# Kernel tuning notes

Measured on AMD Instinct MI355X. Metric: run time of the kernel, lower is better.

## Reference

```python
import jax, jax.numpy as jnp
import numpy as np

N0, N1, N2 = 819200, 81920, 8192
E1, E2 = 819200, 81920
DIN, DH, DOUT = 128, 256, 128


def setup_inputs() -> dict:
    key = jax.random.key(0)
    ks = jax.random.split(key, 12)
    inp = {
        "x": jax.random.normal(ks[0], (N0, DIN), dtype=jnp.float32),
        "src1": jax.random.randint(ks[1], (E1,), 0, N0, dtype=jnp.int32),
        "dst1": jax.random.randint(ks[2], (E1,), 0, N1, dtype=jnp.int32),
        "src2": jax.random.randint(ks[3], (E2,), 0, N1, dtype=jnp.int32),
        "dst2": jax.random.randint(ks[4], (E2,), 0, N2, dtype=jnp.int32),
        "n1": N1,
        "n2": N2,
        # SAGEConv layer 1 params (lin_l has bias, lin_r no bias, PyG default)
        "w1l": jax.random.normal(ks[5], (DIN, DH), dtype=jnp.float32) / np.sqrt(DIN),
        "b1": jnp.zeros((DH,), dtype=jnp.float32),
        "w1r": jax.random.normal(ks[6], (DIN, DH), dtype=jnp.float32) / np.sqrt(DIN),
        # SAGEConv layer 2 params
        "w2l": jax.random.normal(ks[7], (DH, DOUT), dtype=jnp.float32) / np.sqrt(DH),
        "b2": jnp.zeros((DOUT,), dtype=jnp.float32),
        "w2r": jax.random.normal(ks[8], (DH, DOUT), dtype=jnp.float32) / np.sqrt(DH),
    }
    return inp


def _sage_conv(x_src, x_dst, src, dst, n_dst, wl, bl, wr):
    # mean aggregation of neighbor (source) features into destinations
    msg = x_src[src]                                            # [E, d]
    agg = jax.ops.segment_sum(msg, dst, num_segments=n_dst)     # [n_dst, d]
    cnt = jax.ops.segment_sum(jnp.ones((dst.shape[0],), msg.dtype), dst,
                              num_segments=n_dst)               # [n_dst]
    mean = agg / jnp.maximum(cnt, 1.0)[:, None]
    return mean @ wl + bl + x_dst @ wr


def reference(x, src1, dst1, src2, dst2, n1, n2, w1l, b1, w1r, w2l, b2, w2r):
    # layer 1 (eval mode: dropout is a no-op)
    h = _sage_conv(x, x[:n1], src1, dst1, n1, w1l, b1, w1r)     # [n1, DH]
    h = jax.nn.relu(h)
    # layer 2
    out = _sage_conv(h, h[:n2], src2, dst2, n2, w2l, b2, w2r)   # [n2, DOUT]
    return out
```

## Files before the change

kernel.cpp:

```cpp
#include <hip/hip_runtime.h>

constexpr int cN0 = 819200, cN1 = 81920, cN2 = 8192;
constexpr int cE1 = 819200, cE2 = 81920;
constexpr int cDIN = 128, cDH = 256, cDOUT = 128;

typedef __attribute__((ext_vector_type(8))) short bf16x8;
typedef __attribute__((ext_vector_type(4))) float f32x4;
typedef __attribute__((ext_vector_type(8))) unsigned short u16x8;

__device__ __forceinline__ unsigned short f2bf(float f) {
    unsigned u = __builtin_bit_cast(unsigned, f);
    u += 0x7FFF + ((u >> 16) & 1);
    return (unsigned short)(u >> 16);
}
__device__ __forceinline__ float bf2f(unsigned short s) {
    unsigned u = ((unsigned)s) << 16;
    return __builtin_bit_cast(float, u);
}

__global__ __launch_bounds__(256) void hist_k(
    const int* __restrict__ dst, int* __restrict__ hist, int nedges)
{
    int e = blockIdx.x * 256 + threadIdx.x;
    if (e < nedges) atomicAdd(&hist[dst[e]], 1);
}

__global__ __launch_bounds__(1024) void partial_k(
    const int* __restrict__ a, int* __restrict__ part)
{
    const int tid = threadIdx.x, lane = tid & 63, wid = tid >> 6;
    int v = a[blockIdx.x * 1024 + tid];
    #pragma unroll
    for (int off = 32; off; off >>= 1) v += __shfl_xor(v, off);
    __shared__ int ws[16];
    if (lane == 0) ws[wid] = v;
    __syncthreads();
    if (tid == 0) {
        int s = 0;
        #pragma unroll
        for (int i = 0; i < 16; ++i) s += ws[i];
        part[blockIdx.x] = s;
    }
}

__global__ __launch_bounds__(128) void scanp_k(int* __restrict__ part)
{
    const int tid = threadIdx.x, lane = tid & 63, wid = tid >> 6;
    int v = (tid < 80) ? part[tid] : 0;
    int incl = v;
    #pragma unroll
    for (int off = 1; off < 64; off <<= 1) {
        int t = __shfl_up(incl, off, 64);
        if (lane >= off) incl += t;
    }
    __shared__ int w0;
    if (wid == 0 && lane == 63) w0 = incl;
    __syncthreads();
    int pre = wid ? w0 : 0;
    if (tid < 80) part[tid] = pre + incl - v;
}

__global__ __launch_bounds__(1024) void final_k(
    int* __restrict__ a, const int* __restrict__ part)
{
    const int tid = threadIdx.x, lane = tid & 63, wid = tid >> 6;
    const int g = blockIdx.x * 1024 + tid;
    int v = a[g];
    int incl = v;
    #pragma unroll
    for (int off = 1; off < 64; off <<= 1) {
        int t = __shfl_up(incl, off, 64);
        if (lane >= off) incl += t;
    }
    __shared__ int ws[16];
    if (lane == 63) ws[wid] = incl;
    __syncthreads();
    int pre = 0;
    #pragma unroll
    for (int i = 0; i < 16; ++i) if (i < wid) pre += ws[i];
    a[g] = part[blockIdx.x] + pre + incl - v;
}

__global__ __launch_bounds__(1024) void scan_k(int* __restrict__ a, int n)
{
    __shared__ int wsum[16];
    __shared__ int carry_s;
    const int tid = threadIdx.x;
    const int lane = tid & 63, wid = tid >> 6;
    if (tid == 0) carry_s = 0;
    __syncthreads();
    for (int base = 0; base < n; base += 1024) {
        int v = (base + tid < n) ? a[base + tid] : 0;
        int incl = v;
        #pragma unroll
        for (int off = 1; off < 64; off <<= 1) {
            int t = __shfl_up(incl, off, 64);
            if (lane >= off) incl += t;
        }
        if (lane == 63) wsum[wid] = incl;
        __syncthreads();
        int wpre = 0;
        #pragma unroll
        for (int w = 0; w < 15; ++w) if (w < wid) wpre += wsum[w];
        int c = carry_s;
        if (base + tid < n) a[base + tid] = c + wpre + incl - v;
        __syncthreads();
        if (tid == 1023) carry_s = c + wpre + incl;
    }
}

__global__ __launch_bounds__(256) void build_k(
    const int* __restrict__ src, const int* __restrict__ dst,
    int* __restrict__ cursor, int* __restrict__ eidx, int nedges)
{
    int e = blockIdx.x * 256 + threadIdx.x;
    if (e < nedges) {
        int p = atomicAdd(&cursor[dst[e]], 1);
        eidx[p] = src[e];
    }
}

__global__ __launch_bounds__(256) void agg1_k(
    const float* __restrict__ x, const int* __restrict__ cursor,
    const int* __restrict__ eidx, unsigned short* __restrict__ A1)
{
    const int row = blockIdx.x * 4 + (threadIdx.x >> 6);
    const int lane = threadIdx.x & 63;
    const int half = lane >> 5, li = lane & 31;
    const int start = row ? cursor[row - 1] : 0;
    const int end = cursor[row];
    float ax = 0.f, ay = 0.f, az = 0.f, aw = 0.f;
    for (int e = start + half; e < end; e += 2) {
        const int s = eidx[e];
        float4 v = *reinterpret_cast<const float4*>(x + (size_t)s * cDIN + li * 4);
        ax += v.x; ay += v.y; az += v.z; aw += v.w;
    }
    ax += __shfl_xor(ax, 32);
    ay += __shfl_xor(ay, 32);
    az += __shfl_xor(az, 32);
    aw += __shfl_xor(aw, 32);
    const float inv = 1.0f / fmaxf((float)(end - start), 1.0f);
    if (half == 0) {
        ushort4 o;
        o.x = f2bf(ax * inv); o.y = f2bf(ay * inv);
        o.z = f2bf(az * inv); o.w = f2bf(aw * inv);
        *reinterpret_cast<ushort4*>(A1 + (size_t)row * 256 + li * 4) = o;
    }
    float2 xv = *reinterpret_cast<const float2*>(x + (size_t)row * cDIN + lane * 2);
    unsigned pk = (unsigned)f2bf(xv.x) | ((unsigned)f2bf(xv.y) << 16);
    *reinterpret_cast<unsigned*>(A1 + (size_t)row * 256 + 128 + lane * 2) = pk;
}

__global__ __launch_bounds__(256) void agg2_k(
    const unsigned short* __restrict__ h, const int* __restrict__ cursor,
    const int* __restrict__ eidx, unsigned short* __restrict__ A2)
{
    const int row = blockIdx.x * 4 + (threadIdx.x >> 6);
    const int lane = threadIdx.x & 63;
    const int half = lane >> 5, li = lane & 31;
    const int start = row ? cursor[row - 1] : 0;
    const int end = cursor[row];
    float acc[8] = {};
    for (int e = start + half; e < end; e += 2) {
        const int s = eidx[e];
        u16x8 v = *reinterpret_cast<const u16x8*>(h + (size_t)s * cDH + li * 8);
        #pragma unroll
        for (int i = 0; i < 8; ++i) acc[i] += bf2f(v[i]);
    }
    #pragma unroll
    for (int i = 0; i < 8; ++i) acc[i] += __shfl_xor(acc[i], 32);
    const float inv = 1.0f / fmaxf((float)(end - start), 1.0f);
    if (half == 0) {
        u16x8 o;
        #pragma unroll
        for (int i = 0; i < 8; ++i) o[i] = f2bf(acc[i] * inv);
        *reinterpret_cast<u16x8*>(A2 + (size_t)row * 512 + li * 8) = o;
    }
}

__global__ __launch_bounds__(256) void wprep_k(
    const float* __restrict__ w1l, const float* __restrict__ w1r,
    const float* __restrict__ w2l, const float* __restrict__ w2r,
    unsigned short* __restrict__ W1c, unsigned short* __restrict__ W2c)
{
    int id = blockIdx.x * 256 + threadIdx.x;
    if (id < 256 * 256) {
        int n = id >> 8, k = id & 255;
        float v = (k < 128) ? w1l[k * 256 + n] : w1r[(k - 128) * 256 + n];
        W1c[n * 256 + k] = f2bf(v);
    } else {
        int id2 = id - 256 * 256;
        int n = id2 >> 9, k = id2 & 511;
        float v = (k < 256) ? w2l[k * 128 + n] : w2r[(k - 256) * 128 + n];
        W2c[n * 512 + k] = f2bf(v);
    }
}

template<int K, int N, bool L1MODE>
__global__ __launch_bounds__(256) void mfma_gemm_k(
    const unsigned short* __restrict__ A, const unsigned short* __restrict__ Bt,
    const float* __restrict__ bias,
    unsigned short* __restrict__ hout, unsigned short* __restrict__ a2r,
    float* __restrict__ fout)
{
    constexpr int LD = 40;
    __shared__ unsigned short As[128 * LD];
    __shared__ unsigned short Bs[128 * LD];

    const int tid = threadIdx.x;
    const int l = tid & 63, w = tid >> 6;
    const int q = l >> 4, r16 = l & 15;
    const int wr0 = (w >> 1) * 64, wc0 = (w & 1) * 64;
    const int n0 = blockIdx.x * 128, row0 = blockIdx.y * 128;

    const f32x4 zero = {0.f, 0.f, 0.f, 0.f};
    f32x4 acc[4][4];
    #pragma unroll
    for (int m = 0; m < 4; ++m)
        #pragma unroll
        for (int n = 0; n < 4; ++n) acc[m][n] = zero;

    for (int k0 = 0; k0 < K; k0 += 32) {
        __syncthreads();
        #pragma unroll
        for (int c = 0; c < 2; ++c) {
            int z = tid + c * 256;
            int r = z >> 2, o16 = z & 3;
            bf16x8 av = *reinterpret_cast<const bf16x8*>(A + (size_t)(row0 + r) * K + k0 + o16 * 8);
            bf16x8 bv = *reinterpret_cast<const bf16x8*>(Bt + (size_t)(n0 + r) * K + k0 + o16 * 8);
            *reinterpret_cast<bf16x8*>(As + r * LD + o16 * 8) = av;
            *reinterpret_cast<bf16x8*>(Bs + r * LD + o16 * 8) = bv;
        }
        __syncthreads();
        bf16x8 af[4], bg[4];
        #pragma unroll
        for (int m = 0; m < 4; ++m)
            af[m] = *reinterpret_cast<const bf16x8*>(As + (wr0 + 16 * m + r16) * LD + q * 8);
        #pragma unroll
        for (int n = 0; n < 4; ++n)
            bg[n] = *reinterpret_cast<const bf16x8*>(Bs + (wc0 + 16 * n + r16) * LD + q * 8);
        #pragma unroll
        for (int m = 0; m < 4; ++m)
            #pragma unroll
            for (int n = 0; n < 4; ++n)
                acc[m][n] = __builtin_amdgcn_mfma_f32_16x16x32_bf16(af[m], bg[n], acc[m][n], 0, 0, 0);
    }

    #pragma unroll
    for (int n = 0; n < 4; ++n) {
        const int col = n0 + wc0 + 16 * n + r16;
        const float bv = bias[col];
        #pragma unroll
        for (int m = 0; m < 4; ++m) {
            #pragma unroll
            for (int j = 0; j < 4; ++j) {
                const int row = row0 + wr0 + 16 * m + 4 * q + j;
                float v = acc[m][n][j] + bv;
                if (L1MODE) {
                    v = fmaxf(v, 0.f);
                    unsigned short b = f2bf(v);
                    hout[(size_t)row * N + col] = b;
                    if (row < cN2) a2r[(size_t)row * 512 + col] = b;
                } else {
                    fout[(size_t)row * N + col] = v;
                }
            }
        }
    }
}

extern "C" void kernel_launch(void* const* d_in, const int* in_sizes, int n_in,
                              void* d_out, int out_size, void* d_ws, size_t ws_size,
                              hipStream_t stream)
{
    const float* x    = (const float*)d_in[0];
    const int*   src1 = (const int*)d_in[1];
    const int*   dst1 = (const int*)d_in[2];
    const int*   src2 = (const int*)d_in[3];
    const int*   dst2 = (const int*)d_in[4];
    const float* w1l  = (const float*)d_in[7];
    const float* b1   = (const float*)d_in[8];
    const float* w1r  = (const float*)d_in[9];
    const float* w2l  = (const float*)d_in[10];
    const float* b2   = (const float*)d_in[11];
    const float* w2r  = (const float*)d_in[12];
    float* out = (float*)d_out;

    unsigned short* A1  = (unsigned short*)d_ws;
    unsigned short* h   = A1 + (size_t)cN1 * 256;
    unsigned short* A2  = h + (size_t)cN1 * 256;
    unsigned short* W1c = A2 + (size_t)cN2 * 512;
    unsigned short* W2c = W1c + 256 * 256;
    int* offs1 = (int*)(W2c + 128 * 512);
    int* eidx1 = offs1 + cN1;
    int* offs2 = eidx1 + cE1;
    int* eidx2 = offs2 + cN2;
    int* part1 = eidx2 + cE2;

    hipMemsetAsync(offs1, 0, (size_t)cN1 * sizeof(int), stream);
    hipMemsetAsync(offs2, 0, (size_t)cN2 * sizeof(int), stream);

    wprep_k<<<(256 * 256 + 128 * 512) / 256, 256, 0, stream>>>(w1l, w1r, w2l, w2r, W1c, W2c);

    hist_k<<<cE1 / 256, 256, 0, stream>>>(dst1, offs1, cE1);
    partial_k<<<cN1 / 1024, 1024, 0, stream>>>(offs1, part1);
    scanp_k<<<1, 128, 0, stream>>>(part1);
    final_k<<<cN1 / 1024, 1024, 0, stream>>>(offs1, part1);
    build_k<<<cE1 / 256, 256, 0, stream>>>(src1, dst1, offs1, eidx1, cE1);
    agg1_k<<<cN1 / 4, 256, 0, stream>>>(x, offs1, eidx1, A1);

    mfma_gemm_k<256, 256, true><<<dim3(2, cN1 / 128), 256, 0, stream>>>(
        A1, W1c, b1, h, A2 + 256, nullptr);

    hist_k<<<cE2 / 256, 256, 0, stream>>>(dst2, offs2, cE2);
    scan_k<<<1, 1024, 0, stream>>>(offs2, cN2);
    build_k<<<cE2 / 256, 256, 0, stream>>>(src2, dst2, offs2, eidx2, cE2);
    agg2_k<<<cN2 / 4, 256, 0, stream>>>(h, offs2, eidx2, A2);

    mfma_gemm_k<512, 128, false><<<dim3(1, cN2 / 128), 256, 0, stream>>>(
        A2, W2c, b2, nullptr, nullptr, out);
}
```

Before: 280.7 us.

## Merge both graph CSR builds and feed GEMMs from split left/right sources

The CSR construction for both layers now runs in one pass. A single offsets array covers both layers, and the histogram, scan and build kernels handle both edge sets together, with the memsets folded into the weight-prep kernel. This removes the serial single-block scan and several launches. The GEMMs no longer need concatenated A buffers: the left half is read from the bf16 mean and the right half directly from x (converted from fp32 on load) or from h. Layer 2 uses 64-row tiles to launch more blocks, and the aggregation kernels split each row's edges across 4 lane groups instead of 2.

```diff
diff --git a/kernel.cpp b/kernel.cpp
--- a/kernel.cpp
+++ b/kernel.cpp
@@ -3,6 +3,7 @@
 constexpr int cN0 = 819200, cN1 = 81920, cN2 = 8192;
 constexpr int cE1 = 819200, cE2 = 81920;
 constexpr int cDIN = 128, cDH = 256, cDOUT = 128;
+constexpr int cNOFF = cN1 + cN2;
 
 typedef __attribute__((ext_vector_type(8))) short bf16x8;
 typedef __attribute__((ext_vector_type(4))) float f32x4;
@@ -18,11 +19,39 @@
     return __builtin_bit_cast(float, u);
 }
 
+__global__ __launch_bounds__(256) void setup_k(
+    int* __restrict__ offs,
+    const float* __restrict__ w1l, const float* __restrict__ w1r,
+    const float* __restrict__ w2l, const float* __restrict__ w2r,
+    unsigned short* __restrict__ W1c, unsigned short* __restrict__ W2c)
+{
+    int id = blockIdx.x * 256 + threadIdx.x;
+    if (id < cNOFF) { offs[id] = 0; return; }
+    int t = id - cNOFF;
+    if (t < 256 * 256) {
+        int n = t >> 8, k = t & 255;
+        float v = (k < 128) ? w1l[k * 256 + n] : w1r[(k - 128) * 256 + n];
+        W1c[n * 256 + k] = f2bf(v);
+    } else {
+        t -= 256 * 256;
+        if (t < 128 * 512) {
+            int n = t >> 9, k = t & 511;
+            float v = (k < 256) ? w2l[k * 128 + n] : w2r[(k - 256) * 128 + n];
+            W2c[n * 512 + k] = f2bf(v);
+        }
+    }
+}
+
 __global__ __launch_bounds__(256) void hist_k(
-    const int* __restrict__ dst, int* __restrict__ hist, int nedges)
+    const int* __restrict__ dst1, const int* __restrict__ dst2,
+    int* __restrict__ offs)
 {
     int e = blockIdx.x * 256 + threadIdx.x;
-    if (e < nedges) atomicAdd(&hist[dst[e]], 1);
+    if (e < cE1) atomicAdd(&offs[dst1[e]], 1);
+    else {
+        int e2 = e - cE1;
+        if (e2 < cE2) atomicAdd(&offs[cN1 + dst2[e2]], 1);
+    }
 }
 
 __global__ __launch_bounds__(1024) void partial_k(
@@ -46,7 +75,7 @@
 __global__ __launch_bounds__(128) void scanp_k(int* __restrict__ part)
 {
     const int tid = threadIdx.x, lane = tid & 63, wid = tid >> 6;
-    int v = (tid < 80) ? part[tid] : 0;
+    int v = (tid < 88) ? part[tid] : 0;
     int incl = v;
     #pragma unroll
     for (int off = 1; off < 64; off <<= 1) {
@@ -57,7 +86,7 @@
     if (wid == 0 && lane == 63) w0 = incl;
     __syncthreads();
     int pre = wid ? w0 : 0;
-    if (tid < 80) part[tid] = pre + incl - v;
+    if (tid < 88) part[tid] = pre + incl - v;
 }
 
 __global__ __launch_bounds__(1024) void final_k(
@@ -78,189 +107,176 @@
     int pre = 0;
     #pragma unroll
     for (int i = 0; i < 16; ++i) if (i < wid) pre += ws[i];
-    a[g] = part[blockIdx.x] + pre + incl - v;
-}
-
-__global__ __launch_bounds__(1024) void scan_k(int* __restrict__ a, int n)
-{
-    __shared__ int wsum[16];
-    __shared__ int carry_s;
-    const int tid = threadIdx.x;
-    const int lane = tid & 63, wid = tid >> 6;
-    if (tid == 0) carry_s = 0;
-    __syncthreads();
-    for (int base = 0; base < n; base += 1024) {
-        int v = (base + tid < n) ? a[base + tid] : 0;
-        int incl = v;
-        #pragma unroll
-        for (int off = 1; off < 64; off <<= 1) {
-            int t = __shfl_up(incl, off, 64);
-            if (lane >= off) incl += t;
-        }
-        if (lane == 63) wsum[wid] = incl;
-        __syncthreads();
-        int wpre = 0;
-        #pragma unroll
-        for (int w = 0; w < 15; ++w) if (w < wid) wpre += wsum[w];
-        int c = carry_s;
-        if (base + tid < n) a[base + tid] = c + wpre + incl - v;
-        __syncthreads();
-        if (tid == 1023) carry_s = c + wpre + incl;
-    }
+    int r = part[blockIdx.x] + pre + incl - v;
+    if (g >= cN1) r -= cE1;
+    a[g] = r;
 }
 
 __global__ __launch_bounds__(256) void build_k(
-    const int* __restrict__ src, const int* __restrict__ dst,
-    int* __restrict__ cursor, int* __restrict__ eidx, int nedges)
+    const int* __restrict__ src1, const int* __restrict__ dst1,
+    const int* __restrict__ src2, const int* __restrict__ dst2,
+    int* __restrict__ offs, int* __restrict__ eidx1, int* __restrict__ eidx2)
 {
     int e = blockIdx.x * 256 + threadIdx.x;
-    if (e < nedges) {
-        int p = atomicAdd(&cursor[dst[e]], 1);
-        eidx[p] = src[e];
+    if (e < cE1) {
+        int p = atomicAdd(&offs[dst1[e]], 1);
+        eidx1[p] = src1[e];
+    } else {
+        int e2 = e - cE1;
+        if (e2 < cE2) {
+            int p = atomicAdd(&offs[cN1 + dst2[e2]], 1);
+            eidx2[p] = src2[e2];
+        }
     }
 }
 
 __global__ __launch_bounds__(256) void agg1_k(
     const float* __restrict__ x, const int* __restrict__ cursor,
-    const int* __restrict__ eidx, unsigned short* __restrict__ A1)
+    const int* __restrict__ eidx, unsigned short* __restrict__ mean1)
 {
     const int row = blockIdx.x * 4 + (threadIdx.x >> 6);
     const int lane = threadIdx.x & 63;
-    const int half = lane >> 5, li = lane & 31;
-    const int start = row ? cursor[row - 1] : 0;
-    const int end = cursor[row];
-    float ax = 0.f, ay = 0.f, az = 0.f, aw = 0.f;
-    for (int e = start + half; e < end; e += 2) {
-        const int s = eidx[e];
-        float4 v = *reinterpret_cast<const float4*>(x + (size_t)s * cDIN + li * 4);
-        ax += v.x; ay += v.y; az += v.z; aw += v.w;
-    }
-    ax += __shfl_xor(ax, 32);
-    ay += __shfl_xor(ay, 32);
-    az += __shfl_xor(az, 32);
-    aw += __shfl_xor(aw, 32);
-    const float inv = 1.0f / fmaxf((float)(end - start), 1.0f);
-    if (half == 0) {
-        ushort4 o;
-        o.x = f2bf(ax * inv); o.y = f2bf(ay * inv);
-        o.z = f2bf(az * inv); o.w = f2bf(aw * inv);
-        *reinterpret_cast<ushort4*>(A1 + (size_t)row * 256 + li * 4) = o;
-    }
-    float2 xv = *reinterpret_cast<const float2*>(x + (size_t)row * cDIN + lane * 2);
-    unsigned pk = (unsigned)f2bf(xv.x) | ((unsigned)f2bf(xv.y) << 16);
-    *reinterpret_cast<unsigned*>(A1 + (size_t)row * 256 + 128 + lane * 2) = pk;
-}
-
-__global__ __launch_bounds__(256) void agg2_k(
-    const unsigned short* __restrict__ h, const int* __restrict__ cursor,
-    const int* __restrict__ eidx, unsigned short* __restrict__ A2)
-{
-    const int row = blockIdx.x * 4 + (threadIdx.x >> 6);
-    const int lane = threadIdx.x & 63;
-    const int half = lane >> 5, li = lane & 31;
+    const int g = lane >> 4, li = lane & 15;
     const int start = row ? cursor[row - 1] : 0;
     const int end = cursor[row];
     float acc[8] = {};
-    for (int e = start + half; e < end; e += 2) {
+    for (int e = start + g; e < end; e += 4) {
         const int s = eidx[e];
-        u16x8 v = *reinterpret_cast<const u16x8*>(h + (size_t)s * cDH + li * 8);
-        #pragma unroll
-        for (int i = 0; i < 8; ++i) acc[i] += bf2f(v[i]);
-    }
-    #pragma unroll
-    for (int i = 0; i < 8; ++i) acc[i] += __shfl_xor(acc[i], 32);
-    const float inv = 1.0f / fmaxf((float)(end - start), 1.0f);
-    if (half == 0) {
+        const float4* p = reinterpret_cast<const float4*>(x + (size_t)s * cDIN + li * 8);
+        float4 a = p[0], b = p[1];
+        acc[0] += a.x; acc[1] += a.y; acc[2] += a.z; acc[3] += a.w;
+        acc[4] += b.x; acc[5] += b.y; acc[6] += b.z; acc[7] += b.w;
+    }
+    #pragma unroll
+    for (int i = 0; i < 8; ++i) {
+        acc[i] += __shfl_xor(acc[i], 16);
+        acc[i] += __shfl_xor(acc[i], 32);
+    }
+    if (g == 0) {
+        const float inv = 1.0f / fmaxf((float)(end - start), 1.0f);
         u16x8 o;
         #pragma unroll
         for (int i = 0; i < 8; ++i) o[i] = f2bf(acc[i] * inv);
-        *reinterpret_cast<u16x8*>(A2 + (size_t)row * 512 + li * 8) = o;
-    }
-}
-
-__global__ __launch_bounds__(256) void wprep_k(
-    const float* __restrict__ w1l, const float* __restrict__ w1r,
-    const float* __restrict__ w2l, const float* __restrict__ w2r,
-    unsigned short* __restrict__ W1c, unsigned short* __restrict__ W2c)
-{
-    int id = blockIdx.x * 256 + threadIdx.x;
-    if (id < 256 * 256) {
-        int n = id >> 8, k = id & 255;
-        float v = (k < 128) ? w1l[k * 256 + n] : w1r[(k - 128) * 256 + n];
-        W1c[n * 256 + k] = f2bf(v);
-    } else {
-        int id2 = id - 256 * 256;
-        int n = id2 >> 9, k = id2 & 511;
-        float v = (k < 256) ? w2l[k * 128 + n] : w2r[(k - 256) * 128 + n];
-        W2c[n * 512 + k] = f2bf(v);
-    }
-}
-
-template<int K, int N, bool L1MODE>
+        *reinterpret_cast<u16x8*>(mean1 + (size_t)row * cDIN + li * 8) = o;
+    }
+}
+
+__global__ __launch_bounds__(256) void agg2_k(
+    const unsigned short* __restrict__ h, const int* __restrict__ cursor,
+    const int* __restrict__ eidx, unsigned short* __restrict__ mean2)
+{
+    const int row = blockIdx.x * 4 + (threadIdx.x >> 6);
+    const int lane = threadIdx.x & 63;
+    const int g = lane >> 4, li = lane & 15;
+    const int start = row ? cursor[row - 1] : 0;
+    const int end = cursor[row];
+    float acc[16] = {};
+    for (int e = start + g; e < end; e += 4) {
+        const int s = eidx[e];
+        const u16x8* p = reinterpret_cast<const u16x8*>(h + (size_t)s * cDH + li * 16);
+        u16x8 a = p[0], b = p[1];
+        #pragma unroll
+        for (int i = 0; i < 8; ++i) { acc[i] += bf2f(a[i]); acc[8 + i] += bf2f(b[i]); }
+    }
+    #pragma unroll
+    for (int i = 0; i < 16; ++i) {
+        acc[i] += __shfl_xor(acc[i], 16);
+        acc[i] += __shfl_xor(acc[i], 32);
+    }
+    if (g == 0) {
+        const float inv = 1.0f / fmaxf((float)(end - start), 1.0f);
+        u16x8 o0, o1;
+        #pragma unroll
+        for (int i = 0; i < 8; ++i) { o0[i] = f2bf(acc[i] * inv); o1[i] = f2bf(acc[8 + i] * inv); }
+        u16x8* q = reinterpret_cast<u16x8*>(mean2 + (size_t)row * cDH + li * 16);
+        q[0] = o0; q[1] = o1;
+    }
+}
+
+template<int K, int N, int TM, bool RIGHT_F32, bool L1MODE>
 __global__ __launch_bounds__(256) void mfma_gemm_k(
-    const unsigned short* __restrict__ A, const unsigned short* __restrict__ Bt,
-    const float* __restrict__ bias,
-    unsigned short* __restrict__ hout, unsigned short* __restrict__ a2r,
-    float* __restrict__ fout)
-{
+    const unsigned short* __restrict__ Aleft, const void* __restrict__ Aright,
+    const unsigned short* __restrict__ Bt, const float* __restrict__ bias,
+    unsigned short* __restrict__ hout, float* __restrict__ fout)
+{
+    constexpr int KL = K / 2;
     constexpr int LD = 40;
-    __shared__ unsigned short As[128 * LD];
+    constexpr int WR = 4;
+    constexpr int WC = (TM == 128) ? 4 : 2;
+    __shared__ unsigned short As[TM * LD];
     __shared__ unsigned short Bs[128 * LD];
 
     const int tid = threadIdx.x;
     const int l = tid & 63, w = tid >> 6;
     const int q = l >> 4, r16 = l & 15;
-    const int wr0 = (w >> 1) * 64, wc0 = (w & 1) * 64;
-    const int n0 = blockIdx.x * 128, row0 = blockIdx.y * 128;
+    const int wr0 = (TM == 128) ? (w >> 1) * 64 : 0;
+    const int wc0 = (TM == 128) ? (w & 1) * 64 : w * 32;
+    const int n0 = blockIdx.x * 128, row0 = blockIdx.y * TM;
 
     const f32x4 zero = {0.f, 0.f, 0.f, 0.f};
-    f32x4 acc[4][4];
-    #pragma unroll
-    for (int m = 0; m < 4; ++m)
-        #pragma unroll
-        for (int n = 0; n < 4; ++n) acc[m][n] = zero;
+    f32x4 acc[WR][WC];
+    #pragma unroll
+    for (int m = 0; m < WR; ++m)
+        #pragma unroll
+        for (int n = 0; n < WC; ++n) acc[m][n] = zero;
 
     for (int k0 = 0; k0 < K; k0 += 32) {
+        const bool left = (k0 < KL);
         __syncthreads();
+        #pragma unroll
+        for (int c = 0; c < (TM * 4) / 256; ++c) {
+            int z = tid + c * 256;
+            int r = z >> 2, o16 = z & 3;
+            bf16x8 av;
+            if (left) {
+                av = *reinterpret_cast<const bf16x8*>(Aleft + (size_t)(row0 + r) * KL + k0 + o16 * 8);
+            } else if (RIGHT_F32) {
+                const float* p = (const float*)Aright + (size_t)(row0 + r) * KL + (k0 - KL) + o16 * 8;
+                float4 u = *reinterpret_cast<const float4*>(p);
+                float4 v = *reinterpret_cast<const float4*>(p + 4);
+                av[0] = (short)f2bf(u.x); av[1] = (short)f2bf(u.y);
+                av[2] = (short)f2bf(u.z); av[3] = (short)f2bf(u.w);
+                av[4] = (short)f2bf(v.x); av[5] = (short)f2bf(v.y);
+                av[6] = (short)f2bf(v.z); av[7] = (short)f2bf(v.w);
+            } else {
+                av = *reinterpret_cast<const bf16x8*>((const unsigned short*)Aright + (size_t)(row0 + r) * KL + (k0 - KL) + o16 * 8);
+            }
+            *reinterpret_cast<bf16x8*>(As + r * LD + o16 * 8) = av;
+        }
         #pragma unroll
         for (int c = 0; c < 2; ++c) {
             int z = tid + c * 256;
             int r = z >> 2, o16 = z & 3;
-            bf16x8 av = *reinterpret_cast<const bf16x8*>(A + (size_t)(row0 + r) * K + k0 + o16 * 8);
             bf16x8 bv = *reinterpret_cast<const bf16x8*>(Bt + (size_t)(n0 + r) * K + k0 + o16 * 8);
-            *reinterpret_cast<bf16x8*>(As + r * LD + o16 * 8) = av;
             *reinterpret_cast<bf16x8*>(Bs + r * LD + o16 * 8) = bv;
         }
         __syncthreads();
-        bf16x8 af[4], bg[4];
-        #pragma unroll
-        for (int m = 0; m < 4; ++m)
+        bf16x8 af[WR], bg[WC];
+        #pragma unroll
+        for (int m = 0; m < WR; ++m)
             af[m] = *reinterpret_cast<const bf16x8*>(As + (wr0 + 16 * m + r16) * LD + q * 8);
         #pragma unroll
-        for (int n = 0; n < 4; ++n)
+        for (int n = 0; n < WC; ++n)
             bg[n] = *reinterpret_cast<const bf16x8*>(Bs + (wc0 + 16 * n + r16) * LD + q * 8);
         #pragma unroll
-        for (int m = 0; m < 4; ++m)
+        for (int m = 0; m < WR; ++m)
             #pragma unroll
-            for (int n = 0; n < 4; ++n)
+            for (int n = 0; n < WC; ++n)
                 acc[m][n] = __builtin_amdgcn_mfma_f32_16x16x32_bf16(af[m], bg[n], acc[m][n], 0, 0, 0);
     }
 
     #pragma unroll
-    for (int n = 0; n < 4; ++n) {
+    for (int n = 0; n < WC; ++n) {
         const int col = n0 + wc0 + 16 * n + r16;
         const float bv = bias[col];
         #pragma unroll
-        for (int m = 0; m < 4; ++m) {
+        for (int m = 0; m < WR; ++m) {
             #pragma unroll
             for (int j = 0; j < 4; ++j) {
                 const int row = row0 + wr0 + 16 * m + 4 * q + j;
                 float v = acc[m][n][j] + bv;
                 if (L1MODE) {
-                    v = fmaxf(v, 0.f);
-                    unsigned short b = f2bf(v);
-                    hout[(size_t)row * N + col] = b;
-                    if (row < cN2) a2r[(size_t)row * 512 + col] = b;
+                    hout[(size_t)row * N + col] = f2bf(fmaxf(v, 0.f));
                 } else {
                     fout[(size_t)row * N + col] = v;
                 }
@@ -286,37 +302,33 @@
     const float* w2r  = (const float*)d_in[12];
     float* out = (float*)d_out;
 
-    unsigned short* A1  = (unsigned short*)d_ws;
-    unsigned short* h   = A1 + (size_t)cN1 * 256;
-    unsigned short* A2  = h + (size_t)cN1 * 256;
-    unsigned short* W1c = A2 + (size_t)cN2 * 512;
-    unsigned short* W2c = W1c + 256 * 256;
-    int* offs1 = (int*)(W2c + 128 * 512);
-    int* eidx1 = offs1 + cN1;
-    int* offs2 = eidx1 + cE1;
-    int* eidx2 = offs2 + cN2;
-    int* part1 = eidx2 + cE2;
-
-    hipMemsetAsync(offs1, 0, (size_t)cN1 * sizeof(int), stream);
-    hipMemsetAsync(offs2, 0, (size_t)cN2 * sizeof(int), stream);
-
-    wprep_k<<<(256 * 256 + 128 * 512) / 256, 256, 0, stream>>>(w1l, w1r, w2l, w2r, W1c, W2c);
-
-    hist_k<<<cE1 / 256, 256, 0, stream>>>(dst1, offs1, cE1);
-    partial_k<<<cN1 / 1024, 1024, 0, stream>>>(offs1, part1);
-    scanp_k<<<1, 128, 0, stream>>>(part1);
-    final_k<<<cN1 / 1024, 1024, 0, stream>>>(offs1, part1);
-    build_k<<<cE1 / 256, 256, 0, stream>>>(src1, dst1, offs1, eidx1, cE1);
-    agg1_k<<<cN1 / 4, 256, 0, stream>>>(x, offs1, eidx1, A1);
-
-    mfma_gemm_k<256, 256, true><<<dim3(2, cN1 / 128), 256, 0, stream>>>(
-        A1, W1c, b1, h, A2 + 256, nullptr);
-
-    hist_k<<<cE2 / 256, 256, 0, stream>>>(dst2, offs2, cE2);
-    scan_k<<<1, 1024, 0, stream>>>(offs2, cN2);
-    build_k<<<cE2 / 256, 256, 0, stream>>>(src2, dst2, offs2, eidx2, cE2);
-    agg2_k<<<cN2 / 4, 256, 0, stream>>>(h, offs2, eidx2, A2);
-
-    mfma_gemm_k<512, 128, false><<<dim3(1, cN2 / 128), 256, 0, stream>>>(
-        A2, W2c, b2, nullptr, nullptr, out);
-}
+    unsigned short* mean1 = (unsigned short*)d_ws;
+    unsigned short* h     = mean1 + (size_t)cN1 * cDIN;
+    unsigned short* mean2 = h + (size_t)cN1 * cDH;
+    unsigned short* W1c   = mean2 + (size_t)cN2 * cDH;
+    unsigned short* W2c   = W1c + 256 * 256;
+    int* offs  = (int*)(W2c + 128 * 512);
+    int* eidx1 = offs + cNOFF;
+    int* eidx2 = eidx1 + cE1;
+    int* part  = eidx2 + cE2;
+
+    {
+        int total = cNOFF + 256 * 256 + 128 * 512;
+        setup_k<<<(total + 255) / 256, 256, 0, stream>>>(offs, w1l, w1r, w2l, w2r, W1c, W2c);
+    }
+    hist_k<<<(cE1 + cE2) / 256, 256, 0, stream>>>(dst1, dst2, offs);
+    partial_k<<<cNOFF / 1024, 1024, 0, stream>>>(offs, part);
+    scanp_k<<<1, 128, 0, stream>>>(part);
+    final_k<<<cNOFF / 1024, 1024, 0, stream>>>(offs, part);
+    build_k<<<(cE1 + cE2) / 256, 256, 0, stream>>>(src1, dst1, src2, dst2, offs, eidx1, eidx2);
+
+    agg1_k<<<cN1 / 4, 256, 0, stream>>>(x, offs, eidx1, mean1);
+
+    mfma_gemm_k<256, 256, 128, true, true><<<dim3(2, cN1 / 128), 256, 0, stream>>>(
+        mean1, (const void*)x, W1c, b1, h, nullptr);
+
+    agg2_k<<<cN2 / 4, 256, 0, stream>>>(h, offs + cN1, eidx2, mean2);
+
+    mfma_gemm_k<512, 128, 64, false, false><<<dim3(1, cN2 / 64), 256, 0, stream>>>(
+        mean2, (const void*)h, W2c, b2, nullptr, out);
+}
```

After: 240.3 us. -14.4%, faster.
